# Optimization experiments

Measured on AMD Instinct MI355X. Metric: run time of the kernel, lower is better.

Reference implementation:

```python
import math
import jax, jax.numpy as jnp
import numpy as np

L, H, E, D = 12, 12, 768, 64   # stack_size, mh_size, embedding_dim, dim_w_matrices
B, S = 4, 512
EPS = 1e-5


def positional_enc(seq_len, model_dim):
    # faithful: power_ind = 10000 XOR int(2*i/dim)
    i = np.arange(model_dim)
    p = np.bitwise_xor(10000, (2 * i) // model_dim).astype(np.float32)
    pos = np.arange(seq_len, dtype=np.float32)[:, None]
    ang = pos / p[None, :]
    pe = np.where(i % 2 == 0, np.sin(ang), np.cos(ang)).astype(np.float32)
    return jnp.asarray(pe)


def layer_norm(x, g, b):
    mu = jnp.mean(x, axis=-1, keepdims=True)
    var = jnp.mean(jnp.square(x - mu), axis=-1, keepdims=True)
    return (x - mu) * jax.lax.rsqrt(var + EPS) * g + b


def encoder(x, wq, wo, g1, b1, fw, fb, g2, b2):
    # x: [B,S,E]; wq: [H,E,D]; wo: [E,H*D]; fw: [E,E] (torch Linear layout)
    bs = x.shape[0] * x.shape[1]
    nb = x.reshape(bs, E)                              # flatten batch (faithful)
    q = jnp.einsum('ne,hed->hnd', nb, wq)              # q == k == v (bug kept)
    scores = jax.nn.softmax(jnp.einsum('hnd,hmd->hnm', q, q) / math.sqrt(D), axis=-1)
    z = jnp.einsum('hnm,hmd->hnd', scores, q)          # [H,BS,D]
    zc = z.reshape(H * D, bs)                          # per-head view(D,-1) + cat
    mh = (wo @ zc).reshape(x.shape)                    # [B,S,E]
    l1 = layer_norm(x + mh, g1, b1)
    ffn = l1 @ fw.T + fb
    return layer_norm(l1 + ffn, g2, b2)


def setup_inputs() -> dict:
    key = jax.random.key(0)
    ks = jax.random.split(key, 8)

    def xavier(k, shape, fan_in, fan_out):
        lim = math.sqrt(6.0 / (fan_in + fan_out))
        return jax.random.uniform(k, shape, jnp.float32, -lim, lim)

    return {
        'tokens': jax.random.normal(ks[0], (B, S, E), jnp.float32),
        'wq':    xavier(ks[1], (L, H, E, D), E, D),
        'wo':    xavier(ks[2], (L, E, H * D), E, H * D),
        'ln1_g': jnp.ones((L, E), jnp.float32),
        'ln1_b': jnp.zeros((L, E), jnp.float32),
        'ffn_w': xavier(ks[3], (L, E, E), E, E),
        'ffn_b': jnp.zeros((L, E), jnp.float32),
        'ln2_g': jnp.ones((L, E), jnp.float32),
        'ln2_b': jnp.zeros((L, E), jnp.float32),
    }


def reference(tokens, wq, wo, ln1_g, ln1_b, ffn_w, ffn_b, ln2_g, ln2_b):
    pe = positional_enc(tokens.shape[1], tokens.shape[2])
    # faithful: layer 0 applied once on pe+tokens, then ALL layers (0 again) in loop
    x = encoder(pe + tokens, wq[0], wo[0], ln1_g[0], ln1_b[0],
                ffn_w[0], ffn_b[0], ln2_g[0], ln2_b[0])
    for l in range(L):
        x = encoder(x, wq[l], wo[l], ln1_g[l], ln1_b[l],
                    ffn_w[l], ffn_b[l], ln2_g[l], ln2_b[l])
    return x
```

## Files before the change

kernel.cpp:

```cpp
#include <hip/hip_runtime.h>
#include <hip/hip_bf16.h>


#define BS_TOK 2048
#define EMB 768
#define NH 12
#define HD 64
#define WQN (12 * NH * EMB * HD)

typedef __attribute__((ext_vector_type(8))) short bf16x8;
typedef __attribute__((ext_vector_type(4))) short bf16x4;
typedef __attribute__((ext_vector_type(4))) float f32x4;

__device__ __forceinline__ short f2bf(float f) {
  union { __hip_bfloat16 h; short s; } u;
  u.h = __float2bfloat16(f);
  return u.s;
}

#define MFMA16(a, b, c) __builtin_amdgcn_mfma_f32_16x16x32_bf16(a, b, c, 0, 0, 0)
#define SW64(r, k) ((r) * 64 + ((((k) >> 3) ^ ((r) & 7)) << 3) + ((k) & 7))

__global__ __launch_bounds__(256) void cvt_weights_kernel(const float* __restrict__ wo,
                                                          const float* __restrict__ fw,
                                                          short* __restrict__ wob,
                                                          short* __restrict__ fwb) {
  const float* src = blockIdx.y ? fw : wo;
  short* dst = blockIdx.y ? fwb : wob;
  int i = (blockIdx.x * 256 + threadIdx.x) * 8;
  float4 a = *(const float4*)(src + i);
  float4 b = *(const float4*)(src + i + 4);
  bf16x8 t;
  t[0] = f2bf(a.x); t[1] = f2bf(a.y); t[2] = f2bf(a.z); t[3] = f2bf(a.w);
  t[4] = f2bf(b.x); t[5] = f2bf(b.y); t[6] = f2bf(b.z); t[7] = f2bf(b.w);
  *(bf16x8*)(dst + i) = t;
}

__global__ __launch_bounds__(256) void wq_trans_kernel(const float* __restrict__ wq,
                                                       short* __restrict__ wqT) {
  __shared__ short T[64 * 64];
  const int et = blockIdx.x;
  const int lh = blockIdx.y;
  const int tid = threadIdx.x;
  const float* src = wq + ((size_t)lh * EMB + et * 64) * HD;
  {
    int r = tid >> 2, c16 = (tid & 3) << 4;
    const float* p = src + r * HD + c16;
    float4 x0 = *(const float4*)(p + 0);
    float4 x1 = *(const float4*)(p + 4);
    float4 x2 = *(const float4*)(p + 8);
    float4 x3 = *(const float4*)(p + 12);
    bf16x8 a, b;
    a[0] = f2bf(x0.x); a[1] = f2bf(x0.y); a[2] = f2bf(x0.z); a[3] = f2bf(x0.w);
    a[4] = f2bf(x1.x); a[5] = f2bf(x1.y); a[6] = f2bf(x1.z); a[7] = f2bf(x1.w);
    b[0] = f2bf(x2.x); b[1] = f2bf(x2.y); b[2] = f2bf(x2.z); b[3] = f2bf(x2.w);
    b[4] = f2bf(x3.x); b[5] = f2bf(x3.y); b[6] = f2bf(x3.z); b[7] = f2bf(x3.w);
    int g = c16 >> 3;
    *(bf16x8*)&T[r * 64 + ((g ^ (r & 7)) << 3)] = a;
    *(bf16x8*)&T[r * 64 + (((g + 1) ^ (r & 7)) << 3)] = b;
  }
  __syncthreads();
  {
    int d = tid >> 2, e16 = (tid & 3) << 4;
    bf16x8 t0, t1;
#pragma unroll
    for (int j = 0; j < 8; ++j) t0[j] = T[SW64(e16 + j, d)];
#pragma unroll
    for (int j = 0; j < 8; ++j) t1[j] = T[SW64(e16 + 8 + j, d)];
    short* q = wqT + ((size_t)lh * HD + d) * EMB + et * 64 + e16;
    *(bf16x8*)(q) = t0;
    *(bf16x8*)(q + 8) = t1;
  }
}

__global__ __launch_bounds__(256) void pe_add_kernel(const float* __restrict__ tok,
                                                     float* __restrict__ X,
                                                     short* __restrict__ Xb) {
  int idx = blockIdx.x * 256 + threadIdx.x;
  int e = idx % EMB;
  int t = idx / EMB;
  int s = t & 511;
  float p = (e < 384) ? 10000.0f : 10001.0f;
  float ang = (float)s / p;
  float pe = (e & 1) ? cosf(ang) : sinf(ang);
  float v = tok[idx] + pe;
  X[idx] = v;
  Xb[idx] = f2bf(v);
}

__device__ __forceinline__ void load64(const short* __restrict__ src, int ld,
                                       int row0, int k0, bf16x8* r, int tid) {
  int rr = tid >> 2, kb = (tid & 3) << 4;
  const short* p = src + (size_t)(row0 + rr) * ld + k0 + kb;
  r[0] = *(const bf16x8*)(p);
  r[1] = *(const bf16x8*)(p + 8);
}
__device__ __forceinline__ void write64(short* dst, const bf16x8* r, int tid) {
  int rr = tid >> 2, g = (tid & 3) << 1;
  *(bf16x8*)&dst[rr * 64 + (((g + 0) ^ (rr & 7)) << 3)] = r[0];
  *(bf16x8*)&dst[rr * 64 + (((g + 1) ^ (rr & 7)) << 3)] = r[1];
}

__device__ __forceinline__ void load128(const short* __restrict__ src, int ld,
                                        int row0, int k0, bf16x8* r, int tid) {
  int rr = tid >> 1, kb = (tid & 1) << 5;
  const short* p = src + (size_t)(row0 + rr) * ld + k0 + kb;
  r[0] = *(const bf16x8*)(p);
  r[1] = *(const bf16x8*)(p + 8);
  r[2] = *(const bf16x8*)(p + 16);
  r[3] = *(const bf16x8*)(p + 24);
}
__device__ __forceinline__ void write128(short* dst, const bf16x8* r, int tid) {
  int rr = tid >> 1, g = (tid & 1) << 2;
#pragma unroll
  for (int i = 0; i < 4; ++i)
    *(bf16x8*)&dst[rr * 64 + (((g + i) ^ (rr & 7)) << 3)] = r[i];
}

__device__ __forceinline__ void load_comb(const float* __restrict__ Op,
                                          const float* __restrict__ Lp,
                                          int k0, int col0, float4* a, float4* b,
                                          float& rl, int tid) {
  const int NB = BS_TOK * EMB;
  const int NHT = NH * BS_TOK;
  int kk = tid >> 2, nb = (tid & 3) << 4;
  size_t base = (size_t)(k0 + kk) * BS_TOK + col0 + nb;
  int hq = (int)(base >> 6);
  rl = 1.0f / (Lp[hq] + Lp[hq + NHT]);
#pragma unroll
  for (int q4 = 0; q4 < 4; ++q4) {
    a[q4] = *(const float4*)(Op + base + q4 * 4);
    b[q4] = *(const float4*)(Op + base + NB + q4 * 4);
  }
}
__device__ __forceinline__ void write_comb(short* dst, const float4* a,
                                           const float4* b, float rl, int tid) {
  int kk = tid >> 2, nb = (tid & 3) << 4;
#pragma unroll
  for (int q4 = 0; q4 < 4; ++q4) {
    dst[SW64(nb + q4 * 4 + 0, kk)] = f2bf((a[q4].x + b[q4].x) * rl);
    dst[SW64(nb + q4 * 4 + 1, kk)] = f2bf((a[q4].y + b[q4].y) * rl);
    dst[SW64(nb + q4 * 4 + 2, kk)] = f2bf((a[q4].z + b[q4].z) * rl);
    dst[SW64(nb + q4 * 4 + 3, kk)] = f2bf((a[q4].w + b[q4].w) * rl);
  }
}

#define GEMM_TILE_COMPUTE(As, Bs, acc)                                              \
  {                                                                                 \
    _Pragma("unroll") for (int s = 0; s < 2; ++s) {                                 \
      int ra = (w << 4) + l15;                                                      \
      bf16x8 af = *(const bf16x8*)&As[ra * 64 + ((((s << 2) + quad) ^ (ra & 7)) << 3)]; \
      _Pragma("unroll") for (int nt = 0; nt < 4; ++nt) {                            \
        int rb = (nt << 4) + l15;                                                   \
        bf16x8 bf = *(const bf16x8*)&Bs[rb * 64 + ((((s << 2) + quad) ^ (rb & 7)) << 3)]; \
        acc[nt] = MFMA16(af, bf, acc[nt]);                                          \
      }                                                                             \
    }                                                                               \
  }

#define GEMM_TILE_COMPUTE2(As, Bs, acc)                                             \
  {                                                                                 \
    _Pragma("unroll") for (int s = 0; s < 2; ++s) {                                 \
      bf16x8 af[2];                                                                 \
      _Pragma("unroll") for (int u = 0; u < 2; ++u) {                               \
        int ra = (w << 5) + (u << 4) + l15;                                         \
        af[u] = *(const bf16x8*)&As[ra * 64 + ((((s << 2) + quad) ^ (ra & 7)) << 3)]; \
      }                                                                             \
      _Pragma("unroll") for (int nt = 0; nt < 4; ++nt) {                            \
        int rb = (nt << 4) + l15;                                                   \
        bf16x8 bf = *(const bf16x8*)&Bs[rb * 64 + ((((s << 2) + quad) ^ (rb & 7)) << 3)]; \
        acc[0][nt] = MFMA16(af[0], bf, acc[0][nt]);                                 \
        acc[1][nt] = MFMA16(af[1], bf, acc[1][nt]);                                 \
      }                                                                             \
    }                                                                               \
  }

__global__ __launch_bounds__(256) void gemm_q_kernel(const short* __restrict__ Xb,
                                                     const short* __restrict__ WqT,
                                                     short* __restrict__ Qo,
                                                     short* __restrict__ Qt) {
  __shared__ short As[64 * 64];
  __shared__ short Bs[64 * 64];
  const int m0 = blockIdx.x * 64;
  const int h = blockIdx.y;
  const int tid = threadIdx.x;
  const int w = tid >> 6, lane = tid & 63, l15 = lane & 15, quad = lane >> 4;
  const short* wqh = WqT + (size_t)h * (HD * EMB);
  f32x4 acc[4] = {(f32x4){0, 0, 0, 0}, (f32x4){0, 0, 0, 0},
                  (f32x4){0, 0, 0, 0}, (f32x4){0, 0, 0, 0}};
  bf16x8 ar[2], br[2];
  load64(Xb, EMB, m0, 0, ar, tid);
  load64(wqh, EMB, 0, 0, br, tid);
  for (int k0 = 0; k0 < EMB; k0 += 64) {
    if (k0) __syncthreads();
    write64(As, ar, tid);
    write64(Bs, br, tid);
    __syncthreads();
    if (k0 + 64 < EMB) {
      load64(Xb, EMB, m0, k0 + 64, ar, tid);
      load64(wqh, EMB, 0, k0 + 64, br, tid);
    }
    GEMM_TILE_COMPUTE(As, Bs, acc);
  }
  __syncthreads();
#pragma unroll
  for (int nt = 0; nt < 4; ++nt)
#pragma unroll
    for (int r = 0; r < 4; ++r)
      As[SW64((w << 4) + (quad << 2) + r, (nt << 4) + l15)] = f2bf(acc[nt][r]);
  __syncthreads();
  {
    int r2 = tid >> 2, kb = (tid & 3) << 4;
    int g = kb >> 3;
    bf16x8 q0v = *(const bf16x8*)&As[r2 * 64 + ((g ^ (r2 & 7)) << 3)];
    bf16x8 q1v = *(const bf16x8*)&As[r2 * 64 + (((g + 1) ^ (r2 & 7)) << 3)];
    short* qo = Qo + (size_t)h * (BS_TOK * HD) + (size_t)(m0 + r2) * HD + kb;
    *(bf16x8*)(qo) = q0v;
    *(bf16x8*)(qo + 8) = q1v;
  }
  {
    int d = tid >> 2, tok0 = (tid & 3) << 4;
    bf16x8 t0, t1;
#pragma unroll
    for (int j = 0; j < 8; ++j) t0[j] = As[SW64(tok0 + j, d)];
#pragma unroll
    for (int j = 0; j < 8; ++j) t1[j] = As[SW64(tok0 + 8 + j, d)];
    short* qt = Qt + (size_t)h * (HD * BS_TOK) + (size_t)d * BS_TOK + m0 + tok0;
    *(bf16x8*)(qt) = t0;
    *(bf16x8*)(qt + 8) = t1;
  }
}

__global__ __launch_bounds__(256) void attn_mfma_kernel(const short* __restrict__ Q,
                                                        const short* __restrict__ Qt,
                                                        float* __restrict__ Opart,
                                                        float* __restrict__ Lpart) {
  __shared__ short Ks[64 * 64];
  __shared__ short Vt[64 * 64];
  __shared__ short Pw[4 * 16 * 64];
  const int h = blockIdx.y;
  const int q0 = blockIdx.x * 64;
  const int kt0 = blockIdx.z * 16;
  const int tid = threadIdx.x;
  const int lane = tid & 63;
  const int wv = tid >> 6;
  const int l15 = lane & 15;
  const int quad = lane >> 4;
  const short* Qh = Q + (size_t)h * (BS_TOK * HD);
  const short* Qth = Qt + (size_t)h * (HD * BS_TOK);
  short* myP = Pw + wv * 16 * 64;

  bf16x8 qf[2];
  {
    const short* qp = Qh + (size_t)(q0 + wv * 16 + l15) * HD + quad * 8;
    qf[0] = *(const bf16x8*)(qp);
    qf[1] = *(const bf16x8*)(qp + 32);
  }

  f32x4 o[4];
  float lpl = 0.f;
#pragma unroll
  for (int r = 0; r < 4; ++r) o[r] = (f32x4){0.f, 0.f, 0.f, 0.f};

  bf16x8 kreg[2], vreg[2];
#pragma unroll
  for (int i = 0; i < 2; ++i) {
    int c = i * 256 + tid;
    kreg[i] = *(const bf16x8*)(Qh + kt0 * 4096 + c * 8);
    vreg[i] = *(const bf16x8*)(Qth + (c >> 3) * BS_TOK + kt0 * 64 + (c & 7) * 8);
  }

  for (int kt = 0; kt < 16; ++kt) {
    __syncthreads();
#pragma unroll
    for (int i = 0; i < 2; ++i) {
      int c = i * 256 + tid, row = c >> 3, g = c & 7;
      *(bf16x8*)&Ks[row * 64 + ((g ^ (row & 7)) << 3)] = kreg[i];
      *(bf16x8*)&Vt[row * 64 + ((g ^ (row & 7)) << 3)] = vreg[i];
    }
    __syncthreads();
    if (kt < 15) {
      int gt = kt0 + kt + 1;
#pragma unroll
      for (int i = 0; i < 2; ++i) {
        int c = i * 256 + tid;
        kreg[i] = *(const bf16x8*)(Qh + gt * 4096 + c * 8);
        vreg[i] = *(const bf16x8*)(Qth + (c >> 3) * BS_TOK + gt * 64 + (c & 7) * 8);
      }
    }

    f32x4 s[4];
    __builtin_amdgcn_s_setprio(1);
#pragma unroll
    for (int ct = 0; ct < 4; ++ct) {
      f32x4 acc = (f32x4){0.f, 0.f, 0.f, 0.f};
#pragma unroll
      for (int ks = 0; ks < 2; ++ks) {
        int row = ct * 16 + l15;
        int c = ks * 4 + quad;
        bf16x8 kf = *(const bf16x8*)(&Ks[row * 64 + ((c ^ (row & 7)) << 3)]);
        acc = MFMA16(kf, qf[ks], acc);
      }
      s[ct] = acc;
    }
    __builtin_amdgcn_s_setprio(0);

#pragma unroll
    for (int ct = 0; ct < 4; ++ct) {
      bf16x4 pv4;
#pragma unroll
      for (int r = 0; r < 4; ++r) {
        float p = exp2f(s[ct][r] * 0.18033688011112042f);
        lpl += p;
        pv4[r] = f2bf(p);
      }
      int g = 2 * ct + (quad >> 1);
      *(bf16x4*)&myP[l15 * 64 + ((g ^ (l15 & 7)) << 3) + ((quad & 1) << 2)] = pv4;
    }

    __builtin_amdgcn_s_setprio(1);
#pragma unroll
    for (int ks = 0; ks < 2; ++ks) {
      int c = ks * 4 + quad;
      bf16x8 pf = *(const bf16x8*)(&myP[l15 * 64 + ((c ^ (l15 & 7)) << 3)]);
#pragma unroll
      for (int dt = 0; dt < 4; ++dt) {
        int row = dt * 16 + l15;
        bf16x8 vf = *(const bf16x8*)(&Vt[row * 64 + ((c ^ (row & 7)) << 3)]);
        o[dt] = MFMA16(pf, vf, o[dt]);
      }
    }
    __builtin_amdgcn_s_setprio(0);
  }

  lpl += __shfl_xor(lpl, 16, 64);
  lpl += __shfl_xor(lpl, 32, 64);

  const int NB = BS_TOK * EMB;
  float* Oh = Opart + (size_t)blockIdx.z * NB + (size_t)h * (BS_TOK * HD);
  float* Lh = Lpart + ((size_t)blockIdx.z * NH + h) * BS_TOK;
  if (quad == 0) Lh[q0 + wv * 16 + l15] = lpl;
#pragma unroll
  for (int r = 0; r < 4; ++r) {
    int qrow = q0 + wv * 16 + quad * 4 + r;
#pragma unroll
    for (int dt = 0; dt < 4; ++dt)
      Oh[(size_t)qrow * HD + dt * 16 + l15] = o[dt][r];
  }
}

__global__ __launch_bounds__(256) void gemm_out_kernel(const short* __restrict__ Wob,
                                                       const float* __restrict__ Op,
                                                       const float* __restrict__ Lp,
                                                       float* __restrict__ Pp) {
  __shared__ short As[128 * 64];
  __shared__ short Bs[64 * 64];
  const int n0 = blockIdx.x * 64;
  const int m0 = blockIdx.y * 128;
  const int kz = blockIdx.z * 384;
  const int tid = threadIdx.x;
  const int w = tid >> 6, lane = tid & 63, l15 = lane & 15, quad = lane >> 4;
  f32x4 acc[2][4] = {};
  bf16x8 ar[4];
  float4 ca[4], cb[4];
  float rl;
  load128(Wob, EMB, m0, kz, ar, tid);
  load_comb(Op, Lp, kz, n0, ca, cb, rl, tid);
  for (int k0 = 0; k0 < 384; k0 += 64) {
    if (k0) __syncthreads();
    write128(As, ar, tid);
    write_comb(Bs, ca, cb, rl, tid);
    __syncthreads();
    if (k0 + 64 < 384) {
      load128(Wob, EMB, m0, kz + k0 + 64, ar, tid);
      load_comb(Op, Lp, kz + k0 + 64, n0, ca, cb, rl, tid);
    }
    GEMM_TILE_COMPUTE2(As, Bs, acc);
  }
  float* P = Pp + (size_t)blockIdx.z * (BS_TOK * EMB);
#pragma unroll
  for (int u = 0; u < 2; ++u)
#pragma unroll
    for (int nt = 0; nt < 4; ++nt)
#pragma unroll
      for (int r = 0; r < 4; ++r)
        P[(size_t)(m0 + (w << 5) + (u << 4) + (quad << 2) + r) * BS_TOK + n0 +
          (nt << 4) + l15] = acc[u][nt][r];
}

__global__ __launch_bounds__(256) void gemm_ffn_kernel(const short* __restrict__ L1b,
                                                       const short* __restrict__ Fwb,
                                                       const float* __restrict__ Fb,
                                                       float* __restrict__ Pp) {
  __shared__ short As[128 * 64];
  __shared__ short Bs[64 * 64];
  const int m0 = blockIdx.x * 128;
  const int n0 = blockIdx.y * 64;
  const int kz = blockIdx.z * 384;
  const int tid = threadIdx.x;
  const int w = tid >> 6, lane = tid & 63, l15 = lane & 15, quad = lane >> 4;
  f32x4 acc[2][4] = {};
  bf16x8 ar[4], br[2];
  load128(L1b, EMB, m0, kz, ar, tid);
  load64(Fwb, EMB, n0, kz, br, tid);
  for (int k0 = 0; k0 < 384; k0 += 64) {
    if (k0) __syncthreads();
    write128(As, ar, tid);
    write64(Bs, br, tid);
    __syncthreads();
    if (k0 + 64 < 384) {
      load128(L1b, EMB, m0, kz + k0 + 64, ar, tid);
      load64(Fwb, EMB, n0, kz + k0 + 64, br, tid);
    }
    GEMM_TILE_COMPUTE2(As, Bs, acc);
  }
  float* P = Pp + (size_t)blockIdx.z * (BS_TOK * EMB);
  const bool addb = (blockIdx.z == 0);
#pragma unroll
  for (int nt = 0; nt < 4; ++nt) {
    float bias = addb ? Fb[n0 + (nt << 4) + l15] : 0.0f;
#pragma unroll
    for (int u = 0; u < 2; ++u)
#pragma unroll
      for (int r = 0; r < 4; ++r)
        P[(size_t)(m0 + (w << 5) + (u << 4) + (quad << 2) + r) * EMB + n0 +
          (nt << 4) + l15] = acc[u][nt][r] + bias;
  }
}

__global__ __launch_bounds__(256) void ln_kernel(const float* __restrict__ Xa,
                                                 const float* __restrict__ P,
                                                 const float* __restrict__ g,
                                                 const float* __restrict__ bb,
                                                 float* __restrict__ Out,
                                                 short* __restrict__ Outb) {
  const int NB = BS_TOK * EMB;
  const int wv = threadIdx.x >> 6, lane = threadIdx.x & 63;
  const int t = blockIdx.x * 4 + wv;
  const float* xa = Xa + (size_t)t * EMB;
  const float* p0 = P + (size_t)t * EMB;
  const float* p1 = p0 + NB;
  float4 v[3];
  float s = 0.f;
#pragma unroll
  for (int i = 0; i < 3; ++i) {
    int e = lane * 4 + i * 256;
    float4 a = *(const float4*)(xa + e);
    float4 b = *(const float4*)(p0 + e);
    float4 c = *(const float4*)(p1 + e);
    v[i].x = a.x + b.x + c.x;
    v[i].y = a.y + b.y + c.y;
    v[i].z = a.z + b.z + c.z;
    v[i].w = a.w + b.w + c.w;
    s += v[i].x + v[i].y + v[i].z + v[i].w;
  }
#pragma unroll
  for (int o = 32; o > 0; o >>= 1) s += __shfl_xor(s, o, 64);
  float mu = s * (1.0f / EMB);
  float q = 0.f;
#pragma unroll
  for (int i = 0; i < 3; ++i) {
    float dx = v[i].x - mu, dy = v[i].y - mu, dz = v[i].z - mu, dw = v[i].w - mu;
    q += dx * dx + dy * dy + dz * dz + dw * dw;
  }
#pragma unroll
  for (int o = 32; o > 0; o >>= 1) q += __shfl_xor(q, o, 64);
  float var = q * (1.0f / EMB);
  float r = rsqrtf(var + 1e-5f);
#pragma unroll
  for (int i = 0; i < 3; ++i) {
    int e = lane * 4 + i * 256;
    float4 gg = *(const float4*)(g + e);
    float4 bv = *(const float4*)(bb + e);
    float4 res;
    res.x = (v[i].x - mu) * r * gg.x + bv.x;
    res.y = (v[i].y - mu) * r * gg.y + bv.y;
    res.z = (v[i].z - mu) * r * gg.z + bv.z;
    res.w = (v[i].w - mu) * r * gg.w + bv.w;
    *(float4*)(Out + (size_t)t * EMB + e) = res;
    bf16x4 ob;
    ob[0] = f2bf(res.x);
    ob[1] = f2bf(res.y);
    ob[2] = f2bf(res.z);
    ob[3] = f2bf(res.w);
    *(bf16x4*)(Outb + (size_t)t * EMB + e) = ob;
  }
}

extern "C" void kernel_launch(void* const* d_in, const int* in_sizes, int n_in,
                              void* d_out, int out_size, void* d_ws, size_t ws_size,
                              hipStream_t stream) {
  const float* tok = (const float*)d_in[0];
  const float* wq = (const float*)d_in[1];
  const float* wo = (const float*)d_in[2];
  const float* g1 = (const float*)d_in[3];
  const float* b1 = (const float*)d_in[4];
  const float* fw = (const float*)d_in[5];
  const float* fb = (const float*)d_in[6];
  const float* g2 = (const float*)d_in[7];
  const float* b2 = (const float*)d_in[8];
  const int NB = BS_TOK * EMB;
  float* bufA = (float*)d_ws;
  float* bufB = bufA + NB;
  float* bufC = bufB + NB;
  float* bufD = bufC + NB;
  float* bufE = bufD + NB;
  float* bufF = bufE + NB;
  short* XbA = (short*)(bufF + NB);
  short* L1b = XbA + NB;
  short* Qbf = L1b + NB;
  short* Qtb = Qbf + NB;
  short* wqTb = Qtb + NB;
  short* wob = wqTb + WQN;
  short* fwb = wob + WQN;
  float* Lpart = (float*)(fwb + WQN);

  cvt_weights_kernel<<<dim3(WQN / (256 * 8), 2), 256, 0, stream>>>(wo, fw, wob, fwb);
  wq_trans_kernel<<<dim3(12, 12 * NH), 256, 0, stream>>>(wq, wqTb);
  pe_add_kernel<<<NB / 256, 256, 0, stream>>>(tok, bufA, XbA);
  for (int it = 0; it < 13; ++it) {
    int l = (it == 0) ? 0 : it - 1;
    gemm_q_kernel<<<dim3(32, NH), 256, 0, stream>>>(
        XbA, wqTb + (size_t)l * (NH * HD * EMB), Qbf, Qtb);
    attn_mfma_kernel<<<dim3(32, NH, 2), 256, 0, stream>>>(Qbf, Qtb, bufE, Lpart);
    gemm_out_kernel<<<dim3(32, 6, 2), 256, 0, stream>>>(
        wob + (size_t)l * (EMB * EMB), bufE, Lpart, bufB);
    ln_kernel<<<BS_TOK / 4, 256, 0, stream>>>(bufA, bufB, g1 + l * EMB, b1 + l * EMB,
                                              bufD, L1b);
    gemm_ffn_kernel<<<dim3(16, 12, 2), 256, 0, stream>>>(
        L1b, fwb + (size_t)l * (EMB * EMB), fb + l * EMB, bufB);
    float* ln2_dst = (it == 12) ? (float*)d_out : bufA;
    ln_kernel<<<BS_TOK / 4, 256, 0, stream>>>(bufD, bufB, g2 + l * EMB, b2 + l * EMB,
                                              ln2_dst, XbA);
  }
}
```

Baseline: 1.165 ms.

## Double-buffer LDS in GEMMs and attention, retile attention to 128 queries with 4-way key split

Converts the Q, output-projection and FFN GEMMs and the attention kernel to double-buffered shared memory, so each iteration needs a single barrier and the next tile is staged while the current one is computed. The attention kernel now processes 128 queries per block with two 16-row subtiles per wave, reusing each K/V fragment for both. The key range is split four ways instead of two, and the output GEMM sums four partial outputs and four denominators. This doubles LDS use, raises register pressure, and increases the partial-output buffer and the reads of it in the output GEMM.

```diff
diff --git a/kernel.cpp b/kernel.cpp
--- a/kernel.cpp
+++ b/kernel.cpp
@@ -20,6 +20,7 @@
 
 #define MFMA16(a, b, c) __builtin_amdgcn_mfma_f32_16x16x32_bf16(a, b, c, 0, 0, 0)
 #define SW64(r, k) ((r) * 64 + ((((k) >> 3) ^ ((r) & 7)) << 3) + ((k) & 7))
+#define BAR() asm volatile("s_waitcnt lgkmcnt(0)\n\ts_barrier" ::: "memory")
 
 __global__ __launch_bounds__(256) void cvt_weights_kernel(const float* __restrict__ wo,
                                                           const float* __restrict__ fw,
@@ -119,29 +120,33 @@
 
 __device__ __forceinline__ void load_comb(const float* __restrict__ Op,
                                           const float* __restrict__ Lp,
-                                          int k0, int col0, float4* a, float4* b,
+                                          int k0, int col0, float4 a[4][4],
                                           float& rl, int tid) {
   const int NB = BS_TOK * EMB;
   const int NHT = NH * BS_TOK;
   int kk = tid >> 2, nb = (tid & 3) << 4;
   size_t base = (size_t)(k0 + kk) * BS_TOK + col0 + nb;
   int hq = (int)(base >> 6);
-  rl = 1.0f / (Lp[hq] + Lp[hq + NHT]);
+  rl = 1.0f / ((Lp[hq] + Lp[hq + NHT]) + (Lp[hq + 2 * NHT] + Lp[hq + 3 * NHT]));
+#pragma unroll
+  for (int z = 0; z < 4; ++z)
+#pragma unroll
+    for (int q4 = 0; q4 < 4; ++q4)
+      a[z][q4] = *(const float4*)(Op + base + (size_t)z * NB + q4 * 4);
+}
+__device__ __forceinline__ void write_comb(short* dst, const float4 a[4][4],
+                                           float rl, int tid) {
+  int kk = tid >> 2, nb = (tid & 3) << 4;
 #pragma unroll
   for (int q4 = 0; q4 < 4; ++q4) {
-    a[q4] = *(const float4*)(Op + base + q4 * 4);
-    b[q4] = *(const float4*)(Op + base + NB + q4 * 4);
-  }
-}
-__device__ __forceinline__ void write_comb(short* dst, const float4* a,
-                                           const float4* b, float rl, int tid) {
-  int kk = tid >> 2, nb = (tid & 3) << 4;
-#pragma unroll
-  for (int q4 = 0; q4 < 4; ++q4) {
-    dst[SW64(nb + q4 * 4 + 0, kk)] = f2bf((a[q4].x + b[q4].x) * rl);
-    dst[SW64(nb + q4 * 4 + 1, kk)] = f2bf((a[q4].y + b[q4].y) * rl);
-    dst[SW64(nb + q4 * 4 + 2, kk)] = f2bf((a[q4].z + b[q4].z) * rl);
-    dst[SW64(nb + q4 * 4 + 3, kk)] = f2bf((a[q4].w + b[q4].w) * rl);
+    dst[SW64(nb + q4 * 4 + 0, kk)] =
+        f2bf(((a[0][q4].x + a[1][q4].x) + (a[2][q4].x + a[3][q4].x)) * rl);
+    dst[SW64(nb + q4 * 4 + 1, kk)] =
+        f2bf(((a[0][q4].y + a[1][q4].y) + (a[2][q4].y + a[3][q4].y)) * rl);
+    dst[SW64(nb + q4 * 4 + 2, kk)] =
+        f2bf(((a[0][q4].z + a[1][q4].z) + (a[2][q4].z + a[3][q4].z)) * rl);
+    dst[SW64(nb + q4 * 4 + 3, kk)] =
+        f2bf(((a[0][q4].w + a[1][q4].w) + (a[2][q4].w + a[3][q4].w)) * rl);
   }
 }
 
@@ -179,41 +184,49 @@
                                                      const short* __restrict__ WqT,
                                                      short* __restrict__ Qo,
                                                      short* __restrict__ Qt) {
-  __shared__ short As[64 * 64];
-  __shared__ short Bs[64 * 64];
+  __shared__ short As[2][64 * 64];
+  __shared__ short Bs[2][64 * 64];
   const int m0 = blockIdx.x * 64;
   const int h = blockIdx.y;
   const int tid = threadIdx.x;
   const int w = tid >> 6, lane = tid & 63, l15 = lane & 15, quad = lane >> 4;
   const short* wqh = WqT + (size_t)h * (HD * EMB);
-  f32x4 acc[4] = {(f32x4){0, 0, 0, 0}, (f32x4){0, 0, 0, 0},
-                  (f32x4){0, 0, 0, 0}, (f32x4){0, 0, 0, 0}};
+  f32x4 acc[4] = {};
   bf16x8 ar[2], br[2];
   load64(Xb, EMB, m0, 0, ar, tid);
   load64(wqh, EMB, 0, 0, br, tid);
+  write64(As[0], ar, tid);
+  write64(Bs[0], br, tid);
+  load64(Xb, EMB, m0, 64, ar, tid);
+  load64(wqh, EMB, 0, 64, br, tid);
+  BAR();
   for (int k0 = 0; k0 < EMB; k0 += 64) {
-    if (k0) __syncthreads();
-    write64(As, ar, tid);
-    write64(Bs, br, tid);
-    __syncthreads();
+    const int cur = (k0 >> 6) & 1;
+    const short* Ac = As[cur];
+    const short* Bc = Bs[cur];
+    GEMM_TILE_COMPUTE(Ac, Bc, acc);
     if (k0 + 64 < EMB) {
-      load64(Xb, EMB, m0, k0 + 64, ar, tid);
-      load64(wqh, EMB, 0, k0 + 64, br, tid);
-    }
-    GEMM_TILE_COMPUTE(As, Bs, acc);
-  }
-  __syncthreads();
+      write64((short*)As[cur ^ 1], ar, tid);
+      write64((short*)Bs[cur ^ 1], br, tid);
+      if (k0 + 128 < EMB) {
+        load64(Xb, EMB, m0, k0 + 128, ar, tid);
+        load64(wqh, EMB, 0, k0 + 128, br, tid);
+      }
+    }
+    BAR();
+  }
+  short* T = (short*)As[0];
 #pragma unroll
   for (int nt = 0; nt < 4; ++nt)
 #pragma unroll
     for (int r = 0; r < 4; ++r)
-      As[SW64((w << 4) + (quad << 2) + r, (nt << 4) + l15)] = f2bf(acc[nt][r]);
+      T[SW64((w << 4) + (quad << 2) + r, (nt << 4) + l15)] = f2bf(acc[nt][r]);
   __syncthreads();
   {
     int r2 = tid >> 2, kb = (tid & 3) << 4;
     int g = kb >> 3;
-    bf16x8 q0v = *(const bf16x8*)&As[r2 * 64 + ((g ^ (r2 & 7)) << 3)];
-    bf16x8 q1v = *(const bf16x8*)&As[r2 * 64 + (((g + 1) ^ (r2 & 7)) << 3)];
+    bf16x8 q0v = *(const bf16x8*)&T[r2 * 64 + ((g ^ (r2 & 7)) << 3)];
+    bf16x8 q1v = *(const bf16x8*)&T[r2 * 64 + (((g + 1) ^ (r2 & 7)) << 3)];
     short* qo = Qo + (size_t)h * (BS_TOK * HD) + (size_t)(m0 + r2) * HD + kb;
     *(bf16x8*)(qo) = q0v;
     *(bf16x8*)(qo + 8) = q1v;
@@ -222,25 +235,25 @@
     int d = tid >> 2, tok0 = (tid & 3) << 4;
     bf16x8 t0, t1;
 #pragma unroll
-    for (int j = 0; j < 8; ++j) t0[j] = As[SW64(tok0 + j, d)];
-#pragma unroll
-    for (int j = 0; j < 8; ++j) t1[j] = As[SW64(tok0 + 8 + j, d)];
+    for (int j = 0; j < 8; ++j) t0[j] = T[SW64(tok0 + j, d)];
+#pragma unroll
+    for (int j = 0; j < 8; ++j) t1[j] = T[SW64(tok0 + 8 + j, d)];
     short* qt = Qt + (size_t)h * (HD * BS_TOK) + (size_t)d * BS_TOK + m0 + tok0;
     *(bf16x8*)(qt) = t0;
     *(bf16x8*)(qt + 8) = t1;
   }
 }
 
-__global__ __launch_bounds__(256) void attn_mfma_kernel(const short* __restrict__ Q,
-                                                        const short* __restrict__ Qt,
-                                                        float* __restrict__ Opart,
-                                                        float* __restrict__ Lpart) {
-  __shared__ short Ks[64 * 64];
-  __shared__ short Vt[64 * 64];
-  __shared__ short Pw[4 * 16 * 64];
+__global__ __launch_bounds__(256, 3) void attn_mfma_kernel(const short* __restrict__ Q,
+                                                           const short* __restrict__ Qt,
+                                                           float* __restrict__ Opart,
+                                                           float* __restrict__ Lpart) {
+  __shared__ short Ks[2][64 * 64];
+  __shared__ short Vt[2][64 * 64];
+  __shared__ short Pw[4][32 * 64];
   const int h = blockIdx.y;
-  const int q0 = blockIdx.x * 64;
-  const int kt0 = blockIdx.z * 16;
+  const int q0 = blockIdx.x * 128;
+  const int kt0 = blockIdx.z * 8;
   const int tid = threadIdx.x;
   const int lane = tid & 63;
   const int wv = tid >> 6;
@@ -248,113 +261,146 @@
   const int quad = lane >> 4;
   const short* Qh = Q + (size_t)h * (BS_TOK * HD);
   const short* Qth = Qt + (size_t)h * (HD * BS_TOK);
-  short* myP = Pw + wv * 16 * 64;
-
-  bf16x8 qf[2];
-  {
-    const short* qp = Qh + (size_t)(q0 + wv * 16 + l15) * HD + quad * 8;
-    qf[0] = *(const bf16x8*)(qp);
-    qf[1] = *(const bf16x8*)(qp + 32);
-  }
-
-  f32x4 o[4];
-  float lpl = 0.f;
-#pragma unroll
-  for (int r = 0; r < 4; ++r) o[r] = (f32x4){0.f, 0.f, 0.f, 0.f};
+  short* myP = Pw[wv];
+
+  bf16x8 qf[2][2];
+#pragma unroll
+  for (int sub = 0; sub < 2; ++sub) {
+    const short* qp = Qh + (size_t)(q0 + wv * 32 + sub * 16 + l15) * HD + quad * 8;
+    qf[sub][0] = *(const bf16x8*)(qp);
+    qf[sub][1] = *(const bf16x8*)(qp + 32);
+  }
+
+  f32x4 o[2][4] = {};
+  float lpl[2] = {0.f, 0.f};
 
   bf16x8 kreg[2], vreg[2];
 #pragma unroll
   for (int i = 0; i < 2; ++i) {
     int c = i * 256 + tid;
-    kreg[i] = *(const bf16x8*)(Qh + kt0 * 4096 + c * 8);
-    vreg[i] = *(const bf16x8*)(Qth + (c >> 3) * BS_TOK + kt0 * 64 + (c & 7) * 8);
-  }
-
-  for (int kt = 0; kt < 16; ++kt) {
-    __syncthreads();
-#pragma unroll
-    for (int i = 0; i < 2; ++i) {
-      int c = i * 256 + tid, row = c >> 3, g = c & 7;
-      *(bf16x8*)&Ks[row * 64 + ((g ^ (row & 7)) << 3)] = kreg[i];
-      *(bf16x8*)&Vt[row * 64 + ((g ^ (row & 7)) << 3)] = vreg[i];
-    }
-    __syncthreads();
-    if (kt < 15) {
-      int gt = kt0 + kt + 1;
-#pragma unroll
-      for (int i = 0; i < 2; ++i) {
-        int c = i * 256 + tid;
-        kreg[i] = *(const bf16x8*)(Qh + gt * 4096 + c * 8);
-        vreg[i] = *(const bf16x8*)(Qth + (c >> 3) * BS_TOK + gt * 64 + (c & 7) * 8);
-      }
-    }
-
-    f32x4 s[4];
+    kreg[i] = *(const bf16x8*)(Qh + (size_t)kt0 * 4096 + c * 8);
+    vreg[i] = *(const bf16x8*)(Qth + (size_t)(c >> 3) * BS_TOK + kt0 * 64 + (c & 7) * 8);
+  }
+#pragma unroll
+  for (int i = 0; i < 2; ++i) {
+    int c = i * 256 + tid, row = c >> 3, g = c & 7;
+    *(bf16x8*)&Ks[0][row * 64 + ((g ^ (row & 7)) << 3)] = kreg[i];
+    *(bf16x8*)&Vt[0][row * 64 + ((g ^ (row & 7)) << 3)] = vreg[i];
+  }
+#pragma unroll
+  for (int i = 0; i < 2; ++i) {
+    int c = i * 256 + tid;
+    kreg[i] = *(const bf16x8*)(Qh + (size_t)(kt0 + 1) * 4096 + c * 8);
+    vreg[i] = *(const bf16x8*)(Qth + (size_t)(c >> 3) * BS_TOK + (kt0 + 1) * 64 + (c & 7) * 8);
+  }
+  BAR();
+
+  for (int kt = 0; kt < 8; ++kt) {
+    const short* K_ = Ks[kt & 1];
+    const short* V_ = Vt[kt & 1];
+
+    f32x4 s[2][4];
     __builtin_amdgcn_s_setprio(1);
 #pragma unroll
     for (int ct = 0; ct < 4; ++ct) {
-      f32x4 acc = (f32x4){0.f, 0.f, 0.f, 0.f};
-#pragma unroll
-      for (int ks = 0; ks < 2; ++ks) {
-        int row = ct * 16 + l15;
-        int c = ks * 4 + quad;
-        bf16x8 kf = *(const bf16x8*)(&Ks[row * 64 + ((c ^ (row & 7)) << 3)]);
-        acc = MFMA16(kf, qf[ks], acc);
-      }
-      s[ct] = acc;
+      int row = ct * 16 + l15;
+      bf16x8 kf0 = *(const bf16x8*)(&K_[row * 64 + ((quad ^ (row & 7)) << 3)]);
+      bf16x8 kf1 = *(const bf16x8*)(&K_[row * 64 + (((4 + quad) ^ (row & 7)) << 3)]);
+#pragma unroll
+      for (int sub = 0; sub < 2; ++sub) {
+        f32x4 a = (f32x4){0.f, 0.f, 0.f, 0.f};
+        a = MFMA16(kf0, qf[sub][0], a);
+        a = MFMA16(kf1, qf[sub][1], a);
+        s[sub][ct] = a;
+      }
     }
     __builtin_amdgcn_s_setprio(0);
 
 #pragma unroll
-    for (int ct = 0; ct < 4; ++ct) {
-      bf16x4 pv4;
-#pragma unroll
-      for (int r = 0; r < 4; ++r) {
-        float p = exp2f(s[ct][r] * 0.18033688011112042f);
-        lpl += p;
-        pv4[r] = f2bf(p);
-      }
-      int g = 2 * ct + (quad >> 1);
-      *(bf16x4*)&myP[l15 * 64 + ((g ^ (l15 & 7)) << 3) + ((quad & 1) << 2)] = pv4;
+    for (int sub = 0; sub < 2; ++sub) {
+      int prow = sub * 16 + l15;
+#pragma unroll
+      for (int ct = 0; ct < 4; ++ct) {
+        bf16x4 pv4;
+#pragma unroll
+        for (int r = 0; r < 4; ++r) {
+          float p = exp2f(s[sub][ct][r] * 0.18033688011112042f);
+          lpl[sub] += p;
+          pv4[r] = f2bf(p);
+        }
+        int g = 2 * ct + (quad >> 1);
+        *(bf16x4*)&myP[prow * 64 + ((g ^ (prow & 7)) << 3) + ((quad & 1) << 2)] = pv4;
+      }
     }
 
     __builtin_amdgcn_s_setprio(1);
 #pragma unroll
     for (int ks = 0; ks < 2; ++ks) {
       int c = ks * 4 + quad;
-      bf16x8 pf = *(const bf16x8*)(&myP[l15 * 64 + ((c ^ (l15 & 7)) << 3)]);
+      bf16x8 pf0 = *(const bf16x8*)(&myP[l15 * 64 + ((c ^ (l15 & 7)) << 3)]);
+      bf16x8 pf1 = *(const bf16x8*)(&myP[(16 + l15) * 64 + ((c ^ (l15 & 7)) << 3)]);
 #pragma unroll
       for (int dt = 0; dt < 4; ++dt) {
         int row = dt * 16 + l15;
-        bf16x8 vf = *(const bf16x8*)(&Vt[row * 64 + ((c ^ (row & 7)) << 3)]);
-        o[dt] = MFMA16(pf, vf, o[dt]);
+        bf16x8 vf = *(const bf16x8*)(&V_[row * 64 + ((c ^ (row & 7)) << 3)]);
+        o[0][dt] = MFMA16(pf0, vf, o[0][dt]);
+        o[1][dt] = MFMA16(pf1, vf, o[1][dt]);
       }
     }
     __builtin_amdgcn_s_setprio(0);
-  }
-
-  lpl += __shfl_xor(lpl, 16, 64);
-  lpl += __shfl_xor(lpl, 32, 64);
+
+    if (kt + 1 < 8) {
+      short* Kn = (short*)Ks[(kt & 1) ^ 1];
+      short* Vn = (short*)Vt[(kt & 1) ^ 1];
+#pragma unroll
+      for (int i = 0; i < 2; ++i) {
+        int c = i * 256 + tid, row = c >> 3, g = c & 7;
+        *(bf16x8*)&Kn[row * 64 + ((g ^ (row & 7)) << 3)] = kreg[i];
+        *(bf16x8*)&Vn[row * 64 + ((g ^ (row & 7)) << 3)] = vreg[i];
+      }
+      if (kt + 2 < 8) {
+        int gt = kt0 + kt + 2;
+#pragma unroll
+        for (int i = 0; i < 2; ++i) {
+          int c = i * 256 + tid;
+          kreg[i] = *(const bf16x8*)(Qh + (size_t)gt * 4096 + c * 8);
+          vreg[i] = *(const bf16x8*)(Qth + (size_t)(c >> 3) * BS_TOK + gt * 64 + (c & 7) * 8);
+        }
+      }
+    }
+    BAR();
+  }
+
+#pragma unroll
+  for (int sub = 0; sub < 2; ++sub) {
+    lpl[sub] += __shfl_xor(lpl[sub], 16, 64);
+    lpl[sub] += __shfl_xor(lpl[sub], 32, 64);
+  }
 
   const int NB = BS_TOK * EMB;
   float* Oh = Opart + (size_t)blockIdx.z * NB + (size_t)h * (BS_TOK * HD);
   float* Lh = Lpart + ((size_t)blockIdx.z * NH + h) * BS_TOK;
-  if (quad == 0) Lh[q0 + wv * 16 + l15] = lpl;
-#pragma unroll
-  for (int r = 0; r < 4; ++r) {
-    int qrow = q0 + wv * 16 + quad * 4 + r;
-#pragma unroll
-    for (int dt = 0; dt < 4; ++dt)
-      Oh[(size_t)qrow * HD + dt * 16 + l15] = o[dt][r];
-  }
+  if (quad == 0) {
+    Lh[q0 + wv * 32 + l15] = lpl[0];
+    Lh[q0 + wv * 32 + 16 + l15] = lpl[1];
+  }
+#pragma unroll
+  for (int sub = 0; sub < 2; ++sub)
+#pragma unroll
+    for (int r = 0; r < 4; ++r) {
+      int qrow = q0 + wv * 32 + sub * 16 + quad * 4 + r;
+#pragma unroll
+      for (int dt = 0; dt < 4; ++dt)
+        Oh[(size_t)qrow * HD + dt * 16 + l15] = o[sub][dt][r];
+    }
 }
 
 __global__ __launch_bounds__(256) void gemm_out_kernel(const short* __restrict__ Wob,
                                                        const float* __restrict__ Op,
                                                        const float* __restrict__ Lp,
                                                        float* __restrict__ Pp) {
-  __shared__ short As[128 * 64];
-  __shared__ short Bs[64 * 64];
+  __shared__ short As[2][128 * 64];
+  __shared__ short Bs[2][64 * 64];
   const int n0 = blockIdx.x * 64;
   const int m0 = blockIdx.y * 128;
   const int kz = blockIdx.z * 384;
@@ -362,20 +408,29 @@
   const int w = tid >> 6, lane = tid & 63, l15 = lane & 15, quad = lane >> 4;
   f32x4 acc[2][4] = {};
   bf16x8 ar[4];
-  float4 ca[4], cb[4];
+  float4 ca[4][4];
   float rl;
   load128(Wob, EMB, m0, kz, ar, tid);
-  load_comb(Op, Lp, kz, n0, ca, cb, rl, tid);
+  load_comb(Op, Lp, kz, n0, ca, rl, tid);
+  write128((short*)As[0], ar, tid);
+  write_comb((short*)Bs[0], ca, rl, tid);
+  load128(Wob, EMB, m0, kz + 64, ar, tid);
+  load_comb(Op, Lp, kz + 64, n0, ca, rl, tid);
+  BAR();
   for (int k0 = 0; k0 < 384; k0 += 64) {
-    if (k0) __syncthreads();
-    write128(As, ar, tid);
-    write_comb(Bs, ca, cb, rl, tid);
-    __syncthreads();
+    const int cur = (k0 >> 6) & 1;
+    const short* Ac = As[cur];
+    const short* Bc = Bs[cur];
+    GEMM_TILE_COMPUTE2(Ac, Bc, acc);
     if (k0 + 64 < 384) {
-      load128(Wob, EMB, m0, kz + k0 + 64, ar, tid);
-      load_comb(Op, Lp, kz + k0 + 64, n0, ca, cb, rl, tid);
-    }
-    GEMM_TILE_COMPUTE2(As, Bs, acc);
+      write128((short*)As[cur ^ 1], ar, tid);
+      write_comb((short*)Bs[cur ^ 1], ca, rl, tid);
+      if (k0 + 128 < 384) {
+        load128(Wob, EMB, m0, kz + k0 + 128, ar, tid);
+        load_comb(Op, Lp, kz + k0 + 128, n0, ca, rl, tid);
+      }
+    }
+    BAR();
   }
   float* P = Pp + (size_t)blockIdx.z * (BS_TOK * EMB);
 #pragma unroll
@@ -392,8 +447,8 @@
                                                        const short* __restrict__ Fwb,
                                                        const float* __restrict__ Fb,
                                                        float* __restrict__ Pp) {
-  __shared__ short As[128 * 64];
-  __shared__ short Bs[64 * 64];
+  __shared__ short As[2][128 * 64];
+  __shared__ short Bs[2][64 * 64];
   const int m0 = blockIdx.x * 128;
   const int n0 = blockIdx.y * 64;
   const int kz = blockIdx.z * 384;
@@ -403,16 +458,25 @@
   bf16x8 ar[4], br[2];
   load128(L1b, EMB, m0, kz, ar, tid);
   load64(Fwb, EMB, n0, kz, br, tid);
+  write128((short*)As[0], ar, tid);
+  write64((short*)Bs[0], br, tid);
+  load128(L1b, EMB, m0, kz + 64, ar, tid);
+  load64(Fwb, EMB, n0, kz + 64, br, tid);
+  BAR();
   for (int k0 = 0; k0 < 384; k0 += 64) {
-    if (k0) __syncthreads();
-    write128(As, ar, tid);
-    write64(Bs, br, tid);
-    __syncthreads();
+    const int cur = (k0 >> 6) & 1;
+    const short* Ac = As[cur];
+    const short* Bc = Bs[cur];
+    GEMM_TILE_COMPUTE2(Ac, Bc, acc);
     if (k0 + 64 < 384) {
-      load128(L1b, EMB, m0, kz + k0 + 64, ar, tid);
-      load64(Fwb, EMB, n0, kz + k0 + 64, br, tid);
-    }
-    GEMM_TILE_COMPUTE2(As, Bs, acc);
+      write128((short*)As[cur ^ 1], ar, tid);
+      write64((short*)Bs[cur ^ 1], br, tid);
+      if (k0 + 128 < 384) {
+        load128(L1b, EMB, m0, kz + k0 + 128, ar, tid);
+        load64(Fwb, EMB, n0, kz + k0 + 128, br, tid);
+      }
+    }
+    BAR();
   }
   float* P = Pp + (size_t)blockIdx.z * (BS_TOK * EMB);
   const bool addb = (blockIdx.z == 0);
@@ -504,9 +568,8 @@
   float* bufB = bufA + NB;
   float* bufC = bufB + NB;
   float* bufD = bufC + NB;
-  float* bufE = bufD + NB;
-  float* bufF = bufE + NB;
-  short* XbA = (short*)(bufF + NB);
+  float* opart = bufD + NB;
+  short* XbA = (short*)(opart + 4 * (size_t)NB);
   short* L1b = XbA + NB;
   short* Qbf = L1b + NB;
   short* Qtb = Qbf + NB;
@@ -522,9 +585,9 @@
     int l = (it == 0) ? 0 : it - 1;
     gemm_q_kernel<<<dim3(32, NH), 256, 0, stream>>>(
         XbA, wqTb + (size_t)l * (NH * HD * EMB), Qbf, Qtb);
-    attn_mfma_kernel<<<dim3(32, NH, 2), 256, 0, stream>>>(Qbf, Qtb, bufE, Lpart);
+    attn_mfma_kernel<<<dim3(16, NH, 4), 256, 0, stream>>>(Qbf, Qtb, opart, Lpart);
     gemm_out_kernel<<<dim3(32, 6, 2), 256, 0, stream>>>(
-        wob + (size_t)l * (EMB * EMB), bufE, Lpart, bufB);
+        wob + (size_t)l * (EMB * EMB), opart, Lpart, bufB);
     ln_kernel<<<BS_TOK / 4, 256, 0, stream>>>(bufA, bufB, g1 + l * EMB, b1 + l * EMB,
                                               bufD, L1b);
     gemm_ffn_kernel<<<dim3(16, 12, 2), 256, 0, stream>>>(
```

Result: no change. 1.161 ms (-0.3%).
